# Kernel optimization log

Measured on AMD Instinct MI355X. Metric: run time of the kernel, lower is better.

Reference implementation:

```python
import jax, jax.numpy as jnp
import numpy as np

N, P, D, C = 2048, 64, 512, 32   # bs*n_vars, patch_num, hidden_dim, cluster_num
H, DFF, L = 8, 2048, 3           # heads, ffn dim, encoder layers
TEMP = 10.0
EPS = 1e-10
LN_EPS = 1e-5


def setup_inputs() -> dict:
    key = jax.random.key(0)
    ks = jax.random.split(key, 18)
    s = 0.02  # small init to keep activations sane
    inp = {}
    inp["input_series"] = jax.random.normal(ks[0], (N, P, D), jnp.float32)
    pi = jax.random.uniform(ks[1], (C,), jnp.float32) + 0.1
    inp["text_pi"] = pi / pi.sum()
    A = jax.random.uniform(ks[2], (C, C), jnp.float32) + 0.1
    inp["text_A"] = A / A.sum(axis=1, keepdims=True)
    # stacked per-layer TransformerEncoderLayer params (torch post-norm, relu)
    inp["qkv_w"] = jax.random.normal(ks[3], (L, 3 * D, D), jnp.float32) * s
    inp["qkv_b"] = jnp.zeros((L, 3 * D), jnp.float32)
    inp["out_w"] = jax.random.normal(ks[4], (L, D, D), jnp.float32) * s
    inp["out_b"] = jnp.zeros((L, D), jnp.float32)
    inp["ln1_w"] = jnp.ones((L, D), jnp.float32)
    inp["ln1_b"] = jnp.zeros((L, D), jnp.float32)
    inp["ff1_w"] = jax.random.normal(ks[5], (L, DFF, D), jnp.float32) * s
    inp["ff1_b"] = jnp.zeros((L, DFF), jnp.float32)
    inp["ff2_w"] = jax.random.normal(ks[6], (L, D, DFF), jnp.float32) * s
    inp["ff2_b"] = jnp.zeros((L, D), jnp.float32)
    inp["ln2_w"] = jnp.ones((L, D), jnp.float32)
    inp["ln2_b"] = jnp.zeros((L, D), jnp.float32)
    inp["mus"] = jax.random.normal(ks[7], (C, D), jnp.float32)
    return inp


def _layer_norm(x, w, b):
    m = x.mean(axis=-1, keepdims=True)
    v = ((x - m) ** 2).mean(axis=-1, keepdims=True)
    return (x - m) * jax.lax.rsqrt(v + LN_EPS) * w + b


def _encoder_layer(x, qkv_w, qkv_b, out_w, out_b, ln1_w, ln1_b,
                   ff1_w, ff1_b, ff2_w, ff2_b, ln2_w, ln2_b):
    n, p, d = x.shape
    dh = d // H
    qkv = x @ qkv_w.T + qkv_b                       # [n,p,3d]
    q, k, v = jnp.split(qkv, 3, axis=-1)
    def split_heads(t):
        return t.reshape(n, p, H, dh).transpose(0, 2, 1, 3)  # [n,h,p,dh]
    q, k, v = split_heads(q), split_heads(k), split_heads(v)
    scores = jnp.einsum('nhqd,nhkd->nhqk', q, k) / (dh ** 0.5)
    attn = jax.nn.softmax(scores, axis=-1)
    o = jnp.einsum('nhqk,nhkd->nhqd', attn, v)
    o = o.transpose(0, 2, 1, 3).reshape(n, p, d)
    o = o @ out_w.T + out_b
    x = _layer_norm(x + o, ln1_w, ln1_b)            # post-norm
    f = jax.nn.relu(x @ ff1_w.T + ff1_b) @ ff2_w.T + ff2_b
    return _layer_norm(x + f, ln2_w, ln2_b)


def reference(input_series, text_pi, text_A, qkv_w, qkv_b, out_w, out_b,
              ln1_w, ln1_b, ff1_w, ff1_b, ff2_w, ff2_b, ln2_w, ln2_b, mus):
    x = input_series
    for l in range(L):
        x = _encoder_layer(x, qkv_w[l], qkv_b[l], out_w[l], out_b[l],
                           ln1_w[l], ln1_b[l], ff1_w[l], ff1_b[l],
                           ff2_w[l], ff2_b[l], ln2_w[l], ln2_b[l])
    emb_ts = x                                       # [N,P,D]
    # ClusterCenters: softmax of exp(-||x - tanh(mu)||^2 / T)
    mu = jnp.tanh(mus)                               # [C,D]
    dist = ((emb_ts ** 2).sum(-1)[..., None]
            + (mu ** 2).sum(-1)[None, None, :]
            - 2.0 * jnp.einsum('npd,cd->npc', emb_ts, mu))  # [N,P,C]
    z = jnp.exp(-dist / TEMP)
    logits_all = z / z.sum(axis=-1, keepdims=True)
    log_za = jnp.log(logits_all + EPS)               # [N,P,C]
    # sequential HMM-style recursion over patches
    l0 = jax.nn.softmax(jnp.log(text_pi + EPS)[None, :] + log_za[:, 0], axis=-1)
    def step(c, lz):
        c2 = jax.nn.softmax(jnp.log(c @ text_A + EPS) + lz, axis=-1)
        return c2, c2
    _, ys = jax.lax.scan(step, l0, jnp.swapaxes(log_za[:, 1:], 0, 1))  # [P-1,N,C]
    cluster_probs = jnp.concatenate([l0[:, None], jnp.swapaxes(ys, 0, 1)], axis=1)
    entropy_loss = -jnp.sum(cluster_probs * jnp.log(cluster_probs + EPS), axis=-1).mean()
    return (cluster_probs, emb_ts, text_pi, text_A, entropy_loss)
```

## Files before the change

kernel.cpp:

```cpp
#include <hip/hip_runtime.h>
#include <stdint.h>


typedef __bf16 bf16;
typedef __bf16 bf16x2 __attribute__((ext_vector_type(2)));
typedef __bf16 bf16x4 __attribute__((ext_vector_type(4)));
typedef __bf16 bf16x8 __attribute__((ext_vector_type(8)));
typedef float  f32x4  __attribute__((ext_vector_type(4)));
typedef float  f32x2  __attribute__((ext_vector_type(2)));

#define EPSF 1e-10f
#define NROWS 131072L

__device__ __forceinline__ float bflo(uint32_t u){ return __uint_as_float(u << 16); }
__device__ __forceinline__ float bfhi(uint32_t u){ return __uint_as_float(u & 0xffff0000u); }

__device__ __forceinline__ void gload_lds16(const bf16* g, bf16* l){
  __builtin_amdgcn_global_load_lds((const __attribute__((address_space(1))) uint32_t*)g,
                                   (__attribute__((address_space(3))) uint32_t*)l,
                                   16, 0, 0);
}

__global__ void k_f2bf(const float* __restrict__ in, bf16* __restrict__ out, long n){
  const long stride = (long)gridDim.x * blockDim.x * 4;
  for (long i = ((long)blockIdx.x * blockDim.x + threadIdx.x) * 4; i < n; i += stride){
    f32x4 v = *(const f32x4*)(in + i);
    bf16x4 o = { (bf16)v[0], (bf16)v[1], (bf16)v[2], (bf16)v[3] };
    *(bf16x4*)(out + i) = o;
  }
}


#define MFMA_PH(SM, SN)                                                       \
  {                                                                           \
    __builtin_amdgcn_s_setprio(1);                                            \
    _Pragma("unroll")                                                         \
    for (int kk = 0; kk < 2; kk++) {                                          \
      _Pragma("unroll")                                                       \
      for (int i2 = 0; i2 < 4; i2++) {                                        \
        _Pragma("unroll")                                                     \
        for (int j2 = 0; j2 < 2; j2++) {                                      \
          acc[(SM)*4+i2][(SN)*2+j2] = __builtin_amdgcn_mfma_f32_16x16x32_bf16(\
              a[i2][kk], b[SN][j2][kk], acc[(SM)*4+i2][(SN)*2+j2], 0, 0, 0);  \
        }                                                                     \
      }                                                                       \
    }                                                                         \
    __builtin_amdgcn_s_setprio(0);                                            \
  }

#define RD_A(SM)                                                              \
  _Pragma("unroll")                                                           \
  for (int i2 = 0; i2 < 4; i2++) {                                            \
    a[i2][0] = *(const bf16x8*)&Ac[(SM)*8192 + aBase + i2*1024 + sl0];        \
    a[i2][1] = *(const bf16x8*)&Ac[(SM)*8192 + aBase + i2*1024 + sl1];        \
  }

#define RD_B(SN)                                                              \
  _Pragma("unroll")                                                           \
  for (int j2 = 0; j2 < 2; j2++) {                                            \
    b[SN][j2][0] = *(const bf16x8*)&Bc[(SN)*8192 + bBase + j2*1024 + sl0];    \
    b[SN][j2][1] = *(const bf16x8*)&Bc[(SN)*8192 + bBase + j2*1024 + sl1];    \
  }

#define WAITV(N)  asm volatile("s_waitcnt vmcnt(" #N ")" ::: "memory")
#define WAITL0    asm volatile("s_waitcnt lgkmcnt(0)" ::: "memory")
#define BARRIER   { __builtin_amdgcn_s_barrier(); asm volatile("" ::: "memory"); }

#define ZERO_ACC                                                              \
  _Pragma("unroll") for (int zi = 0; zi < 8; zi++)                            \
  _Pragma("unroll") for (int zj = 0; zj < 4; zj++)                            \
    acc[zi][zj] = (f32x4){0.f, 0.f, 0.f, 0.f};

#define EPILOGUE(BME)                                                         \
{                                                                             \
  _Pragma("unroll")                                                           \
  for (int sm = 0; sm < 2; sm++){                                             \
    _Pragma("unroll")                                                         \
    for (int sn = 0; sn < 2; sn++){                                           \
      _Pragma("unroll")                                                       \
      for (int ch = 0; ch < 2; ch++){                                         \
        _Pragma("unroll")                                                     \
        for (int i2 = 0; i2 < 2; i2++){                                       \
          _Pragma("unroll")                                                   \
          for (int j2 = 0; j2 < 2; j2++){                                     \
            _Pragma("unroll")                                                 \
            for (int r = 0; r < 4; r++){                                      \
              float v = acc[sm*4 + ch*2 + i2][sn*2 + j2][r] + bv[sn*2 + j2];  \
              if (RELU) v = fmaxf(v, 0.f);                                    \
              cw[(i2*16 + fg*4 + r)*40 + j2*16 + fr] = (bf16)v;               \
            }                                                                 \
          }                                                                   \
        }                                                                     \
        WAITL0;                                                               \
        const long r0 = (BME) + sm*128 + wr*64 + ch*32;                       \
        const long c0 = bn + sn*128 + wc*32;                                  \
        _Pragma("unroll")                                                     \
        for (int p = 0; p < 2; p++){                                          \
          const int row  = p*16 + (lane >> 2);                                \
          const int colg = (lane & 3)*8;                                      \
          bf16x8 o = *(const bf16x8*)&cw[row*40 + colg];                      \
          *(bf16x8*)&Cb[(r0+row)*ldc + c0 + colg] = o;                        \
        }                                                                     \
        WAITL0;                                                               \
      }                                                                       \
    }                                                                         \
  }                                                                           \
}

template<int RELU>
__global__ __launch_bounds__(512, 2)
void gemm256(const bf16* __restrict__ A, long lda,
             const bf16* __restrict__ W,
             const float* __restrict__ bias,
             bf16* __restrict__ Cb,
             long K, int nbx)
{
  const int tid  = threadIdx.x;
  const int wid  = tid >> 6;
  const int lane = tid & 63;
  const int wr = wid >> 2, wc = wid & 3;
  const long ldc = (long)nbx * 256;

  const unsigned nwg = gridDim.x;
  const unsigned q   = nwg >> 3;
  const unsigned swz = (blockIdx.x & 7) * q + (blockIdx.x >> 3);
  const unsigned bx  = swz % (unsigned)nbx;
  const unsigned by  = swz / (unsigned)nbx;
  const long bm0 = (long)by * 512;
  const long bn  = (long)bx * 256;

  __shared__ __align__(16) bf16 smem[75776];
  bf16* const As0 = smem;
  bf16* const Bs0 = smem + 16384;
  bf16* const As1 = smem + 32768;
  bf16* const Bs1 = smem + 49152;
  bf16* const cw  = smem + 65536 + wid * 1280;

  const int gswz = ((lane & 7) ^ ((lane >> 3) & 7)) * 8;
  const int wsl  = wid * 512;
  const bf16* gA0 = A + (bm0 + wid * 8 + (lane >> 3)) * lda + gswz;
  const bf16* gA1 = gA0 + 256 * lda;
  const bf16* gB  = W + (bn + wid * 8 + (lane >> 3)) * K + gswz;

  const int fr = lane & 15, fg = lane >> 4;
  const int aBase = (wr * 64 + fr) * 64;
  const int bBase = (wc * 32 + fr) * 64;
  const int sl0 = ((0 + fg) ^ (fr & 7)) * 8;
  const int sl1 = ((4 + fg) ^ (fr & 7)) * 8;

  const int nt = (int)(K >> 6);
  const int T  = nt * 2;

  auto issueA = [&](bf16* dst, int ro, int tt){
    const bf16* g = (tt >= nt) ? gA1 : gA0;
    const long kk = (long)(tt >= nt ? tt - nt : tt) << 6;
    gload_lds16(g + (long)ro * lda + kk, dst + ro * 64 + wsl);
  };
  auto issueB = [&](bf16* dst, int ro, int tt){
    const long kk = (long)(tt >= nt ? tt - nt : tt) << 6;
    gload_lds16(gB + (long)ro * K + kk, dst + ro * 64 + wsl);
  };

  f32x4 acc[8][4];
  ZERO_ACC;

  bf16x8 a[4][2];
  bf16x8 b[2][2][2];

  float bv[4];
#pragma unroll
  for (int sn = 0; sn < 2; sn++)
#pragma unroll
    for (int j2 = 0; j2 < 2; j2++)
      bv[sn * 2 + j2] = bias[bn + sn * 128 + wc * 32 + j2 * 16 + fr];

  issueA(As0, 0, 0);   issueA(As0, 64, 0);
  issueB(Bs0, 0, 0);   issueB(Bs0, 64, 0);
  issueA(As0, 128, 0); issueA(As0, 192, 0);
  issueB(Bs0, 128, 0); issueB(Bs0, 192, 0);
  issueA(As1, 0, 1);   issueA(As1, 64, 1);
  issueB(Bs1, 0, 1);   issueB(Bs1, 64, 1);
  WAITV(8);
  BARRIER;

  for (int t = 0; t < T; t++){
    bf16* const Ac = (t & 1) ? As1 : As0;
    bf16* const Bc = (t & 1) ? Bs1 : Bs0;
    bf16* const An = (t & 1) ? As0 : As1;
    bf16* const Bn = (t & 1) ? Bs0 : Bs1;
    const bool s1 = (t + 1 < T);
    const bool s2 = (t + 2 < T);

    RD_A(0); RD_B(0);
    if (s1){ issueA(An, 128, t + 1); issueA(An, 192, t + 1); }
    WAITL0;
    MFMA_PH(0, 0);
    if (s1){ WAITV(6); } else { WAITV(0); }
    BARRIER;

    RD_B(1);
    if (s1){ issueB(Bn, 128, t + 1); issueB(Bn, 192, t + 1); }
    WAITL0;
    MFMA_PH(0, 1);
    BARRIER;

    RD_A(1);
    if (s2){ issueA(Ac, 0, t + 2); issueA(Ac, 64, t + 2); }
    WAITL0;
    MFMA_PH(1, 0);
    BARRIER;

    if (s2){ issueB(Bc, 0, t + 2); issueB(Bc, 64, t + 2); }
    MFMA_PH(1, 1);
    if (s2)      { WAITV(8); }
    else if (s1) { WAITV(4); }
    BARRIER;

    if (t == nt - 1){
      EPILOGUE(bm0);
      ZERO_ACC;
    }
  }

  EPILOGUE(bm0 + 256);
}

__global__ __launch_bounds__(256)
void attention(bf16* __restrict__ qkv)
{
  const int blk = blockIdx.x;
  const long n = blk >> 3;
  const int h  = blk & 7;
  const int tid = threadIdx.x;
  const int wid = tid >> 6, lane = tid & 63;

  __shared__ __align__(16) bf16 Qs[64][72];
  __shared__ __align__(16) bf16 Ks[64][72];
  __shared__ __align__(16) bf16 Vt[64][72];

  bf16* base = qkv + n * 64 * 1536 + h * 64;

  for (int c = tid; c < 512; c += 256){
    const int row = c >> 3, col = (c & 7) * 8, g = c & 7;
    const long go = (long)row * 1536 + col;
    *(bf16x8*)&Qs[row][col] = *(const bf16x8*)(base + go);
    *(bf16x8*)&Ks[row][col] = *(const bf16x8*)(base + 512 + go);
    bf16x8 v = *(const bf16x8*)(base + 1024 + go);
#pragma unroll
    for (int e = 0; e < 8; e++){
      const int vd = (e + g) & 7;
      Vt[col + vd][row] = v[vd];
    }
  }
  __syncthreads();

  const int fr = lane & 15, fg = lane >> 4;
  f32x4 sacc[4];
#pragma unroll
  for (int j = 0; j < 4; j++) sacc[j] = (f32x4){0.f, 0.f, 0.f, 0.f};
#pragma unroll
  for (int ks = 0; ks < 2; ks++){
    bf16x8 aa = *(const bf16x8*)&Qs[wid * 16 + fr][ks * 32 + fg * 8];
#pragma unroll
    for (int j = 0; j < 4; j++){
      bf16x8 bb = *(const bf16x8*)&Ks[j * 16 + fr][ks * 32 + fg * 8];
      sacc[j] = __builtin_amdgcn_mfma_f32_16x16x32_bf16(aa, bb, sacc[j], 0, 0, 0);
    }
  }

  float pv[4][4];
#pragma unroll
  for (int r = 0; r < 4; r++){
    float m = -1e30f;
#pragma unroll
    for (int j = 0; j < 4; j++) m = fmaxf(m, sacc[j][r]);
#pragma unroll
    for (int msk = 1; msk < 16; msk <<= 1) m = fmaxf(m, __shfl_xor(m, msk));
    float s = 0.f;
#pragma unroll
    for (int j = 0; j < 4; j++){
      float p = __expf((sacc[j][r] - m) * 0.125f);
      pv[j][r] = p; s += p;
    }
#pragma unroll
    for (int msk = 1; msk < 16; msk <<= 1) s += __shfl_xor(s, msk);
    const float inv = 1.f / s;
#pragma unroll
    for (int j = 0; j < 4; j++) pv[j][r] *= inv;
  }

#pragma unroll
  for (int j = 0; j < 4; j++)
#pragma unroll
    for (int r = 0; r < 4; r++)
      Qs[wid * 16 + fg * 4 + r][j * 16 + fr] = (bf16)pv[j][r];
  __syncthreads();

  f32x4 oacc[4];
#pragma unroll
  for (int j = 0; j < 4; j++) oacc[j] = (f32x4){0.f, 0.f, 0.f, 0.f};
#pragma unroll
  for (int ks = 0; ks < 2; ks++){
    bf16x8 aa = *(const bf16x8*)&Qs[wid * 16 + fr][ks * 32 + fg * 8];
#pragma unroll
    for (int j = 0; j < 4; j++){
      bf16x8 bb = *(const bf16x8*)&Vt[j * 16 + fr][ks * 32 + fg * 8];
      oacc[j] = __builtin_amdgcn_mfma_f32_16x16x32_bf16(aa, bb, oacc[j], 0, 0, 0);
    }
  }
#pragma unroll
  for (int j = 0; j < 4; j++)
#pragma unroll
    for (int r = 0; r < 4; r++)
      base[(long)(wid * 16 + fg * 4 + r) * 1536 + j * 16 + fr] = (bf16)oacc[j][r];
}

__global__ __launch_bounds__(256)
void resid_ln(const bf16* __restrict__ X, const bf16* __restrict__ O,
              const float* __restrict__ w, const float* __restrict__ b,
              bf16* __restrict__ Y, float* __restrict__ EF)
{
  const int wid = threadIdx.x >> 6, lane = threadIdx.x & 63;
  const long row = (long)blockIdx.x * 4 + wid;
  const uint4 xu = ((const uint4*)(X + row * 512))[lane];
  const uint4 ou = ((const uint4*)(O + row * 512))[lane];
  float s[8];
  s[0] = bflo(xu.x) + bflo(ou.x);  s[1] = bfhi(xu.x) + bfhi(ou.x);
  s[2] = bflo(xu.y) + bflo(ou.y);  s[3] = bfhi(xu.y) + bfhi(ou.y);
  s[4] = bflo(xu.z) + bflo(ou.z);  s[5] = bfhi(xu.z) + bfhi(ou.z);
  s[6] = bflo(xu.w) + bflo(ou.w);  s[7] = bfhi(xu.w) + bfhi(ou.w);
  float sum = 0.f, sq = 0.f;
#pragma unroll
  for (int e = 0; e < 8; e++){ sum += s[e]; sq += s[e] * s[e]; }
#pragma unroll
  for (int m = 1; m < 64; m <<= 1){ sum += __shfl_xor(sum, m); sq += __shfl_xor(sq, m); }
  const float mean = sum * (1.f / 512.f);
  const float var  = sq * (1.f / 512.f) - mean * mean;
  const float rs   = rsqrtf(var + 1e-5f);
  const f32x4 w0 = *(const f32x4*)(w + 8 * lane);
  const f32x4 w1 = *(const f32x4*)(w + 8 * lane + 4);
  const f32x4 b0 = *(const f32x4*)(b + 8 * lane);
  const f32x4 b1 = *(const f32x4*)(b + 8 * lane + 4);
  float o[8];
#pragma unroll
  for (int e = 0; e < 4; e++) o[e]     = (s[e]     - mean) * rs * w0[e] + b0[e];
#pragma unroll
  for (int e = 0; e < 4; e++) o[e + 4] = (s[e + 4] - mean) * rs * w1[e] + b1[e];
  bf16x8 ov = { (bf16)o[0], (bf16)o[1], (bf16)o[2], (bf16)o[3],
                (bf16)o[4], (bf16)o[5], (bf16)o[6], (bf16)o[7] };
  *(bf16x8*)(Y + row * 512 + 8 * lane) = ov;
  if (EF){
    f32x4 e0 = { o[0], o[1], o[2], o[3] };
    f32x4 e1 = { o[4], o[5], o[6], o[7] };
    *(f32x4*)(EF + row * 512 + 8 * lane) = e0;
    *(f32x4*)(EF + row * 512 + 8 * lane + 4) = e1;
  }
}

__global__ __launch_bounds__(256)
void k_mu(const float* __restrict__ mus, bf16* __restrict__ mubf, float* __restrict__ munorm)
{
  const int c = blockIdx.x, tid = threadIdx.x, lane = tid & 63, wid = tid >> 6;
  const f32x2 v = *(const f32x2*)(mus + c * 512 + 2 * tid);
  const float t0 = tanhf(v[0]), t1 = tanhf(v[1]);
  bf16x2 o2 = { (bf16)t0, (bf16)t1 };
  *(bf16x2*)(mubf + c * 512 + 2 * tid) = o2;
  float sq = t0 * t0 + t1 * t1;
#pragma unroll
  for (int m = 1; m < 64; m <<= 1) sq += __shfl_xor(sq, m);
  __shared__ float red[4];
  if (lane == 0) red[wid] = sq;
  __syncthreads();
  if (tid == 0) munorm[c] = red[0] + red[1] + red[2] + red[3];
}

__global__ __launch_bounds__(256)
void cluster_logza(const bf16* __restrict__ X, const bf16* __restrict__ MU,
                   const float* __restrict__ munorm, float* __restrict__ out)
{
  const int tid = threadIdx.x, lane = tid & 63, wid = tid >> 6;
  __shared__ __align__(16) bf16 mus[32][512];
  __shared__ float xs[512];
  __shared__ float red[4];
  __shared__ float dots[32];
  for (int c = tid; c < 2048; c += 256){
    const int r = c >> 6, col = (c & 63) * 8;
    *(bf16x8*)&mus[r][col] = *(const bf16x8*)(MU + r * 512 + col);
  }
  const int cc = tid >> 3, seg = tid & 7;
  const long row0 = (long)blockIdx.x * 16;
  __syncthreads();
  for (int rr = 0; rr < 16; rr++){
    const long row = row0 + rr;
    const uint32_t u = ((const uint32_t*)(X + row * 512))[tid];
    const float aa = bflo(u), bb = bfhi(u);
    xs[2 * tid] = aa; xs[2 * tid + 1] = bb;
    float sq = aa * aa + bb * bb;
#pragma unroll
    for (int m = 1; m < 64; m <<= 1) sq += __shfl_xor(sq, m);
    if (lane == 0) red[wid] = sq;
    __syncthreads();
    const float xn = red[0] + red[1] + red[2] + red[3];
    float p = 0.f;
#pragma unroll
    for (int jj = 0; jj < 8; jj++){
      const int col = jj * 64 + seg * 8;
      bf16x8 m8 = *(const bf16x8*)&mus[cc][col];
      const float* xv = &xs[col];
#pragma unroll
      for (int e = 0; e < 8; e++) p += xv[e] * (float)m8[e];
    }
#pragma unroll
    for (int m = 1; m < 8; m <<= 1) p += __shfl_xor(p, m);
    if (seg == 0) dots[cc] = p;
    __syncthreads();
    if (tid < 32){
      const float dist = xn + munorm[tid] - 2.f * dots[tid];
      const float lg = -dist * 0.1f;
      float mx = lg;
#pragma unroll
      for (int m = 1; m < 32; m <<= 1) mx = fmaxf(mx, __shfl_xor(mx, m, 32));
      const float z = __expf(lg - mx);
      float s = z;
#pragma unroll
      for (int m = 1; m < 32; m <<= 1) s += __shfl_xor(s, m, 32);
      out[row * 32 + tid] = logf(z / s + EPSF);
    }
    __syncthreads();
  }
}

__global__ __launch_bounds__(256)
void k_hmm(const float* __restrict__ lza, const float* __restrict__ pi,
           const float* __restrict__ A, float* __restrict__ cp, float* __restrict__ ent)
{
  __shared__ float As[32][33];
  const int tid = threadIdx.x;
  for (int i = tid; i < 1024; i += 256) As[i >> 5][i & 31] = A[i];
  __syncthreads();
  const int j = tid & 31;
  const long n = (long)blockIdx.x * 8 + (tid >> 5);
  const float* lz = lza + n * 2048;

  float c = logf(pi[j] + EPSF) + lz[j];
  {
    float mx = c;
#pragma unroll
    for (int m = 1; m < 32; m <<= 1) mx = fmaxf(mx, __shfl_xor(mx, m, 32));
    float z = __expf(c - mx), s = z;
#pragma unroll
    for (int m = 1; m < 32; m <<= 1) s += __shfl_xor(s, m, 32);
    c = z / s;
  }
  cp[n * 2048 + j] = c;
  float ea = -c * logf(c + EPSF);

  for (int p = 1; p < 64; p++){
    float y = 0.f;
#pragma unroll
    for (int i = 0; i < 32; i++) y += __shfl(c, i, 32) * As[i][j];
    float t = logf(y + EPSF) + lz[p * 32 + j];
    float mx = t;
#pragma unroll
    for (int m = 1; m < 32; m <<= 1) mx = fmaxf(mx, __shfl_xor(mx, m, 32));
    float z = __expf(t - mx), s = z;
#pragma unroll
    for (int m = 1; m < 32; m <<= 1) s += __shfl_xor(s, m, 32);
    c = z / s;
    cp[n * 2048 + p * 32 + j] = c;
    ea += -c * logf(c + EPSF);
  }
#pragma unroll
  for (int m = 1; m < 32; m <<= 1) ea += __shfl_xor(ea, m, 32);
  if (j == 0) atomicAdd(ent, ea * (1.f / 131072.f));
}

extern "C" void kernel_launch(void* const* d_in, const int* in_sizes, int n_in,
                              void* d_out, int out_size, void* d_ws, size_t ws_size,
                              hipStream_t stream)
{
  (void)in_sizes; (void)n_in; (void)out_size; (void)ws_size;
  const float* in_series = (const float*)d_in[0];
  const float* pi    = (const float*)d_in[1];
  const float* Amat  = (const float*)d_in[2];
  const float* qkv_w = (const float*)d_in[3];
  const float* qkv_b = (const float*)d_in[4];
  const float* out_w = (const float*)d_in[5];
  const float* out_b = (const float*)d_in[6];
  const float* ln1_w = (const float*)d_in[7];
  const float* ln1_b = (const float*)d_in[8];
  const float* ff1_w = (const float*)d_in[9];
  const float* ff1_b = (const float*)d_in[10];
  const float* ff2_w = (const float*)d_in[11];
  const float* ff2_b = (const float*)d_in[12];
  const float* ln2_w = (const float*)d_in[13];
  const float* ln2_b = (const float*)d_in[14];
  const float* mus   = (const float*)d_in[15];

  char* ws = (char*)d_ws;
  bf16* region0 = (bf16*)(ws);
  bf16* xb      = (bf16*)(ws + 536870912L);
  bf16* oproj   = (bf16*)(ws + 671088640L);
  bf16* w_qkv   = (bf16*)(ws + 805306368L);
  bf16* w_out   = (bf16*)(ws + 810024960L);
  bf16* w_ff1   = (bf16*)(ws + 811597824L);
  bf16* w_ff2   = (bf16*)(ws + 817889280L);
  bf16* mubf    = (bf16*)(ws + 824180736L);
  float* munorm = (float*)(ws + 824213504L);
  float* logza  = (float*)(ws);

  float* out_f = (float*)d_out;
  float* cp    = out_f;
  float* emb   = out_f + 4194304L;
  float* o_pi  = out_f + 71303168L;
  float* o_A   = out_f + 71303200L;
  float* o_ent = out_f + 71304224L;

  k_f2bf<<<8192, 256, 0, stream>>>(in_series, xb, 67108864L);
  k_f2bf<<<1024, 256, 0, stream>>>(qkv_w, w_qkv, 2359296L);
  k_f2bf<<<1024, 256, 0, stream>>>(out_w, w_out, 786432L);
  k_f2bf<<<1024, 256, 0, stream>>>(ff1_w, w_ff1, 3145728L);
  k_f2bf<<<1024, 256, 0, stream>>>(ff2_w, w_ff2, 3145728L);
  k_mu<<<32, 256, 0, stream>>>(mus, mubf, munorm);

  for (int l = 0; l < 3; l++){
    gemm256<0><<<1536, 512, 0, stream>>>(xb, 512, w_qkv + (long)l * 786432L,
                                         qkv_b + (long)l * 1536, region0, 512, 6);
    attention<<<16384, 256, 0, stream>>>(region0);
    gemm256<0><<<512, 512, 0, stream>>>(region0, 1536, w_out + (long)l * 262144L,
                                        out_b + (long)l * 512, oproj, 512, 2);
    resid_ln<<<32768, 256, 0, stream>>>(xb, oproj, ln1_w + (long)l * 512,
                                        ln1_b + (long)l * 512, xb, nullptr);
    gemm256<1><<<2048, 512, 0, stream>>>(xb, 512, w_ff1 + (long)l * 1048576L,
                                         ff1_b + (long)l * 2048, region0, 512, 8);
    gemm256<0><<<512, 512, 0, stream>>>(region0, 2048, w_ff2 + (long)l * 1048576L,
                                        ff2_b + (long)l * 512, oproj, 2048, 2);
    resid_ln<<<32768, 256, 0, stream>>>(xb, oproj, ln2_w + (long)l * 512,
                                        ln2_b + (long)l * 512, xb,
                                        (l == 2) ? emb : nullptr);
  }

  cluster_logza<<<8192, 256, 0, stream>>>(xb, mubf, munorm, logza);
  hipMemsetAsync(o_ent, 0, 4, stream);
  k_hmm<<<256, 256, 0, stream>>>(logza, pi, Amat, cp, o_ent);
  hipMemcpyAsync(o_pi, pi, 32 * sizeof(float), hipMemcpyDeviceToDevice, stream);
  hipMemcpyAsync(o_A, Amat, 1024 * sizeof(float), hipMemcpyDeviceToDevice, stream);
}
```

Before: 3.916 ms.

## Fuse cluster log-probabilities with HMM recursion and use grid-stride LN launches

Merges the cluster log-probability kernel and the HMM recursion kernel into one kernel. Each block handles one sequence of 64 patches, keeps the log-probabilities in shared memory and runs the recursion on a single 32-lane group, so the global round trip of the log-probability tensor goes away. The residual-LayerNorm kernel becomes grid-stride with fewer blocks and loads its weights once per wave, and the conversion kernels launch fewer blocks. The trade-off is that the recursion now runs on one 32-lane group per block with the other threads idle, and there are fewer blocks overall.

New measurement: 4.132 ms. +5.5%, slower.

```diff
diff --git a/kernel.cpp b/kernel.cpp
--- a/kernel.cpp
+++ b/kernel.cpp
@@ -321,39 +321,41 @@
               bf16* __restrict__ Y, float* __restrict__ EF)
 {
   const int wid = threadIdx.x >> 6, lane = threadIdx.x & 63;
-  const long row = (long)blockIdx.x * 4 + wid;
-  const uint4 xu = ((const uint4*)(X + row * 512))[lane];
-  const uint4 ou = ((const uint4*)(O + row * 512))[lane];
-  float s[8];
-  s[0] = bflo(xu.x) + bflo(ou.x);  s[1] = bfhi(xu.x) + bfhi(ou.x);
-  s[2] = bflo(xu.y) + bflo(ou.y);  s[3] = bfhi(xu.y) + bfhi(ou.y);
-  s[4] = bflo(xu.z) + bflo(ou.z);  s[5] = bfhi(xu.z) + bfhi(ou.z);
-  s[6] = bflo(xu.w) + bflo(ou.w);  s[7] = bfhi(xu.w) + bfhi(ou.w);
-  float sum = 0.f, sq = 0.f;
-#pragma unroll
-  for (int e = 0; e < 8; e++){ sum += s[e]; sq += s[e] * s[e]; }
-#pragma unroll
-  for (int m = 1; m < 64; m <<= 1){ sum += __shfl_xor(sum, m); sq += __shfl_xor(sq, m); }
-  const float mean = sum * (1.f / 512.f);
-  const float var  = sq * (1.f / 512.f) - mean * mean;
-  const float rs   = rsqrtf(var + 1e-5f);
   const f32x4 w0 = *(const f32x4*)(w + 8 * lane);
   const f32x4 w1 = *(const f32x4*)(w + 8 * lane + 4);
   const f32x4 b0 = *(const f32x4*)(b + 8 * lane);
   const f32x4 b1 = *(const f32x4*)(b + 8 * lane + 4);
-  float o[8];
-#pragma unroll
-  for (int e = 0; e < 4; e++) o[e]     = (s[e]     - mean) * rs * w0[e] + b0[e];
-#pragma unroll
-  for (int e = 0; e < 4; e++) o[e + 4] = (s[e + 4] - mean) * rs * w1[e] + b1[e];
-  bf16x8 ov = { (bf16)o[0], (bf16)o[1], (bf16)o[2], (bf16)o[3],
-                (bf16)o[4], (bf16)o[5], (bf16)o[6], (bf16)o[7] };
-  *(bf16x8*)(Y + row * 512 + 8 * lane) = ov;
-  if (EF){
-    f32x4 e0 = { o[0], o[1], o[2], o[3] };
-    f32x4 e1 = { o[4], o[5], o[6], o[7] };
-    *(f32x4*)(EF + row * 512 + 8 * lane) = e0;
-    *(f32x4*)(EF + row * 512 + 8 * lane + 4) = e1;
+  const long rstep = (long)gridDim.x * 4;
+  for (long row = (long)blockIdx.x * 4 + wid; row < NROWS; row += rstep){
+    const uint4 xu = ((const uint4*)(X + row * 512))[lane];
+    const uint4 ou = ((const uint4*)(O + row * 512))[lane];
+    float s[8];
+    s[0] = bflo(xu.x) + bflo(ou.x);  s[1] = bfhi(xu.x) + bfhi(ou.x);
+    s[2] = bflo(xu.y) + bflo(ou.y);  s[3] = bfhi(xu.y) + bfhi(ou.y);
+    s[4] = bflo(xu.z) + bflo(ou.z);  s[5] = bfhi(xu.z) + bfhi(ou.z);
+    s[6] = bflo(xu.w) + bflo(ou.w);  s[7] = bfhi(xu.w) + bfhi(ou.w);
+    float sum = 0.f, sq = 0.f;
+#pragma unroll
+    for (int e = 0; e < 8; e++){ sum += s[e]; sq += s[e] * s[e]; }
+#pragma unroll
+    for (int m = 1; m < 64; m <<= 1){ sum += __shfl_xor(sum, m); sq += __shfl_xor(sq, m); }
+    const float mean = sum * (1.f / 512.f);
+    const float var  = sq * (1.f / 512.f) - mean * mean;
+    const float rs   = rsqrtf(var + 1e-5f);
+    float o[8];
+#pragma unroll
+    for (int e = 0; e < 4; e++) o[e]     = (s[e]     - mean) * rs * w0[e] + b0[e];
+#pragma unroll
+    for (int e = 0; e < 4; e++) o[e + 4] = (s[e + 4] - mean) * rs * w1[e] + b1[e];
+    bf16x8 ov = { (bf16)o[0], (bf16)o[1], (bf16)o[2], (bf16)o[3],
+                  (bf16)o[4], (bf16)o[5], (bf16)o[6], (bf16)o[7] };
+    *(bf16x8*)(Y + row * 512 + 8 * lane) = ov;
+    if (EF){
+      f32x4 e0 = { o[0], o[1], o[2], o[3] };
+      f32x4 e1 = { o[4], o[5], o[6], o[7] };
+      *(f32x4*)(EF + row * 512 + 8 * lane) = e0;
+      *(f32x4*)(EF + row * 512 + 8 * lane + 4) = e1;
+    }
   }
 }
 
@@ -375,22 +377,29 @@
 }
 
 __global__ __launch_bounds__(256)
-void cluster_logza(const bf16* __restrict__ X, const bf16* __restrict__ MU,
-                   const float* __restrict__ munorm, float* __restrict__ out)
+void k_cluster_hmm(const bf16* __restrict__ X, const bf16* __restrict__ MU,
+                   const float* __restrict__ munorm,
+                   const float* __restrict__ pi, const float* __restrict__ A,
+                   float* __restrict__ cp, float* __restrict__ ent)
 {
   const int tid = threadIdx.x, lane = tid & 63, wid = tid >> 6;
   __shared__ __align__(16) bf16 mus[32][512];
   __shared__ float xs[512];
   __shared__ float red[4];
   __shared__ float dots[32];
+  __shared__ float lzs[64][32];
+  __shared__ float As[32][33];
   for (int c = tid; c < 2048; c += 256){
     const int r = c >> 6, col = (c & 63) * 8;
     *(bf16x8*)&mus[r][col] = *(const bf16x8*)(MU + r * 512 + col);
   }
+  for (int i = tid; i < 1024; i += 256) As[i >> 5][i & 31] = A[i];
   const int cc = tid >> 3, seg = tid & 7;
-  const long row0 = (long)blockIdx.x * 16;
+  const long n = blockIdx.x;
+  const long row0 = n * 64;
   __syncthreads();
-  for (int rr = 0; rr < 16; rr++){
+
+  for (int rr = 0; rr < 64; rr++){
     const long row = row0 + rr;
     const uint32_t u = ((const uint32_t*)(X + row * 512))[tid];
     const float aa = bflo(u), bb = bfhi(u);
@@ -424,55 +433,45 @@
       float s = z;
 #pragma unroll
       for (int m = 1; m < 32; m <<= 1) s += __shfl_xor(s, m, 32);
-      out[row * 32 + tid] = logf(z / s + EPSF);
+      lzs[rr][tid] = logf(z / s + EPSF);
     }
     __syncthreads();
   }
-}
-
-__global__ __launch_bounds__(256)
-void k_hmm(const float* __restrict__ lza, const float* __restrict__ pi,
-           const float* __restrict__ A, float* __restrict__ cp, float* __restrict__ ent)
-{
-  __shared__ float As[32][33];
-  const int tid = threadIdx.x;
-  for (int i = tid; i < 1024; i += 256) As[i >> 5][i & 31] = A[i];
-  __syncthreads();
-  const int j = tid & 31;
-  const long n = (long)blockIdx.x * 8 + (tid >> 5);
-  const float* lz = lza + n * 2048;
-
-  float c = logf(pi[j] + EPSF) + lz[j];
-  {
-    float mx = c;
-#pragma unroll
-    for (int m = 1; m < 32; m <<= 1) mx = fmaxf(mx, __shfl_xor(mx, m, 32));
-    float z = __expf(c - mx), s = z;
-#pragma unroll
-    for (int m = 1; m < 32; m <<= 1) s += __shfl_xor(s, m, 32);
-    c = z / s;
-  }
-  cp[n * 2048 + j] = c;
-  float ea = -c * logf(c + EPSF);
-
-  for (int p = 1; p < 64; p++){
-    float y = 0.f;
-#pragma unroll
-    for (int i = 0; i < 32; i++) y += __shfl(c, i, 32) * As[i][j];
-    float t = logf(y + EPSF) + lz[p * 32 + j];
-    float mx = t;
-#pragma unroll
-    for (int m = 1; m < 32; m <<= 1) mx = fmaxf(mx, __shfl_xor(mx, m, 32));
-    float z = __expf(t - mx), s = z;
-#pragma unroll
-    for (int m = 1; m < 32; m <<= 1) s += __shfl_xor(s, m, 32);
-    c = z / s;
-    cp[n * 2048 + p * 32 + j] = c;
-    ea += -c * logf(c + EPSF);
-  }
-#pragma unroll
-  for (int m = 1; m < 32; m <<= 1) ea += __shfl_xor(ea, m, 32);
-  if (j == 0) atomicAdd(ent, ea * (1.f / 131072.f));
+
+  if (tid < 32){
+    const int j = tid;
+    float c = logf(pi[j] + EPSF) + lzs[0][j];
+    {
+      float mx = c;
+#pragma unroll
+      for (int m = 1; m < 32; m <<= 1) mx = fmaxf(mx, __shfl_xor(mx, m, 32));
+      float z = __expf(c - mx), s = z;
+#pragma unroll
+      for (int m = 1; m < 32; m <<= 1) s += __shfl_xor(s, m, 32);
+      c = z / s;
+    }
+    cp[row0 * 32 + j] = c;
+    float ea = -c * logf(c + EPSF);
+
+    for (int p = 1; p < 64; p++){
+      float y = 0.f;
+#pragma unroll
+      for (int i = 0; i < 32; i++) y += __shfl(c, i, 32) * As[i][j];
+      float t = logf(y + EPSF) + lzs[p][j];
+      float mx = t;
+#pragma unroll
+      for (int m = 1; m < 32; m <<= 1) mx = fmaxf(mx, __shfl_xor(mx, m, 32));
+      float z = __expf(t - mx), s = z;
+#pragma unroll
+      for (int m = 1; m < 32; m <<= 1) s += __shfl_xor(s, m, 32);
+      c = z / s;
+      cp[(row0 + p) * 32 + j] = c;
+      ea += -c * logf(c + EPSF);
+    }
+#pragma unroll
+    for (int m = 1; m < 32; m <<= 1) ea += __shfl_xor(ea, m, 32);
+    if (j == 0) atomicAdd(ent, ea * (1.f / 131072.f));
+  }
 }
 
 extern "C" void kernel_launch(void* const* d_in, const int* in_sizes, int n_in,
@@ -507,7 +506,6 @@
   bf16* w_ff2   = (bf16*)(ws + 817889280L);
   bf16* mubf    = (bf16*)(ws + 824180736L);
   float* munorm = (float*)(ws + 824213504L);
-  float* logza  = (float*)(ws);
 
   float* out_f = (float*)d_out;
   float* cp    = out_f;
@@ -516,11 +514,11 @@
   float* o_A   = out_f + 71303200L;
   float* o_ent = out_f + 71304224L;
 
-  k_f2bf<<<8192, 256, 0, stream>>>(in_series, xb, 67108864L);
-  k_f2bf<<<1024, 256, 0, stream>>>(qkv_w, w_qkv, 2359296L);
-  k_f2bf<<<1024, 256, 0, stream>>>(out_w, w_out, 786432L);
-  k_f2bf<<<1024, 256, 0, stream>>>(ff1_w, w_ff1, 3145728L);
-  k_f2bf<<<1024, 256, 0, stream>>>(ff2_w, w_ff2, 3145728L);
+  k_f2bf<<<2048, 256, 0, stream>>>(in_series, xb, 67108864L);
+  k_f2bf<<<512, 256, 0, stream>>>(qkv_w, w_qkv, 2359296L);
+  k_f2bf<<<512, 256, 0, stream>>>(out_w, w_out, 786432L);
+  k_f2bf<<<512, 256, 0, stream>>>(ff1_w, w_ff1, 3145728L);
+  k_f2bf<<<512, 256, 0, stream>>>(ff2_w, w_ff2, 3145728L);
   k_mu<<<32, 256, 0, stream>>>(mus, mubf, munorm);
 
   for (int l = 0; l < 3; l++){
@@ -529,20 +527,19 @@
     attention<<<16384, 256, 0, stream>>>(region0);
     gemm256<0><<<512, 512, 0, stream>>>(region0, 1536, w_out + (long)l * 262144L,
                                         out_b + (long)l * 512, oproj, 512, 2);
-    resid_ln<<<32768, 256, 0, stream>>>(xb, oproj, ln1_w + (long)l * 512,
-                                        ln1_b + (long)l * 512, xb, nullptr);
+    resid_ln<<<2048, 256, 0, stream>>>(xb, oproj, ln1_w + (long)l * 512,
+                                       ln1_b + (long)l * 512, xb, nullptr);
     gemm256<1><<<2048, 512, 0, stream>>>(xb, 512, w_ff1 + (long)l * 1048576L,
                                          ff1_b + (long)l * 2048, region0, 512, 8);
     gemm256<0><<<512, 512, 0, stream>>>(region0, 2048, w_ff2 + (long)l * 1048576L,
                                         ff2_b + (long)l * 512, oproj, 2048, 2);
-    resid_ln<<<32768, 256, 0, stream>>>(xb, oproj, ln2_w + (long)l * 512,
-                                        ln2_b + (long)l * 512, xb,
-                                        (l == 2) ? emb : nullptr);
-  }
-
-  cluster_logza<<<8192, 256, 0, stream>>>(xb, mubf, munorm, logza);
+    resid_ln<<<2048, 256, 0, stream>>>(xb, oproj, ln2_w + (long)l * 512,
+                                       ln2_b + (long)l * 512, xb,
+                                       (l == 2) ? emb : nullptr);
+  }
+
   hipMemsetAsync(o_ent, 0, 4, stream);
-  k_hmm<<<256, 256, 0, stream>>>(logza, pi, Amat, cp, o_ent);
+  k_cluster_hmm<<<2048, 256, 0, stream>>>(xb, mubf, munorm, pi, Amat, cp, o_ent);
   hipMemcpyAsync(o_pi, pi, 32 * sizeof(float), hipMemcpyDeviceToDevice, stream);
   hipMemcpyAsync(o_A, Amat, 1024 * sizeof(float), hipMemcpyDeviceToDevice, stream);
 }
```
